# Performance work log

Hardware: AMD Instinct MI355X
Metric: run time of the kernel (lower is better)

The kernel has to match this reference:

```python
import jax, jax.numpy as jnp
import numpy as np

B, C, H, W = 8, 128, 64, 64

def setup_inputs() -> dict:
    key = jax.random.key(0)
    ks = jax.random.split(key, 7)
    s = 1.0 / np.sqrt(C)
    return {
        "x": jax.random.normal(ks[0], (B, C, H, W), dtype=jnp.float32),
        "Wq": jax.random.normal(ks[1], (C, C), dtype=jnp.float32) * s,
        "bq": jax.random.normal(ks[2], (C,), dtype=jnp.float32) * 0.01,
        "Wk": jax.random.normal(ks[3], (C, C), dtype=jnp.float32) * s,
        "bk": jax.random.normal(ks[4], (C,), dtype=jnp.float32) * 0.01,
        "Wv": jax.random.normal(ks[5], (C, C), dtype=jnp.float32) * s,
        "bv": jax.random.normal(ks[6], (C,), dtype=jnp.float32) * 0.01,
    }

def reference(x, Wq, bq, Wk, bk, Wv, bv):
    b, c, h, w = x.shape
    n = h * w
    scale = 1.0 / jnp.sqrt(jnp.asarray(c, x.dtype))
    xf = x.reshape(b, c, n)                                   # [B,C,N]
    # 1x1 convs == per-pixel linear layers
    q = jnp.einsum('oc,bcn->bno', Wq, xf) + bq                # [B,N,C]
    k = jnp.einsum('oc,bcn->bcn', Wk, xf) + bk[None, :, None] # [B,C,N]
    v = jnp.einsum('oc,bcn->bno', Wv, xf) + bv                # [B,N,C]
    attn = jax.nn.softmax(jnp.einsum('bnc,bcm->bnm', q, k) * scale, axis=-1)
    out = jnp.einsum('bnm,bmc->bnc', attn, v)                 # [B,N,C]
    return x + out.transpose(0, 2, 1).reshape(b, c, h, w)
```

## Files before the change

### kernel.cpp

```cpp
#include <hip/hip_runtime.h>

#define BB 8
#define CC 128
#define NN 4096

typedef __bf16 bf16x8_t __attribute__((ext_vector_type(8)));
typedef unsigned short u16x8 __attribute__((ext_vector_type(8)));
typedef float f32x4 __attribute__((ext_vector_type(4)));
typedef unsigned int u32x4 __attribute__((ext_vector_type(4)));
typedef __attribute__((address_space(1))) const unsigned int gu32;
typedef __attribute__((address_space(3))) unsigned int lu32;

#define KSCALE 0.12753262456033348f
#define MANCH  8.0f

__device__ __forceinline__ unsigned short f2bf(float f) {
  unsigned int u = __builtin_bit_cast(unsigned int, f);
  u += 0x7fffu + ((u >> 16) & 1u);
  return (unsigned short)(u >> 16);
}

__device__ __forceinline__ float bf2f(unsigned short s) {
  unsigned int u = ((unsigned int)s) << 16;
  return __builtin_bit_cast(float, u);
}

__device__ __forceinline__ unsigned int cvt_pk_bf16(float lo, float hi) {
  unsigned int r;
  asm("v_cvt_pk_bf16_f32 %0, %1, %2" : "=v"(r) : "v"(lo), "v"(hi));
  return r;
}

__device__ __forceinline__ float fexp2(float x) {
  float r;
  asm("v_exp_f32 %0, %1" : "=v"(r) : "v"(x));
  return r;
}

__device__ __forceinline__ f32x4 mfma16(u16x8 a, u16x8 b, f32x4 c) {
  return __builtin_amdgcn_mfma_f32_16x16x32_bf16(
      __builtin_bit_cast(bf16x8_t, a), __builtin_bit_cast(bf16x8_t, b), c, 0, 0, 0);
}

__global__ void prep(const float* __restrict__ Wq, const float* __restrict__ Wv,
                     const float* __restrict__ Wk,
                     unsigned short* __restrict__ Qwb, unsigned short* __restrict__ Vwb,
                     float* __restrict__ csk) {
  if (blockIdx.x < 64) {
    const int i = blockIdx.x * 256 + threadIdx.x;
    Qwb[i] = f2bf(Wq[i] * KSCALE);
    Vwb[i] = f2bf(Wv[i]);
  } else if (threadIdx.x < CC) {
    const int c = threadIdx.x;
    float s = 0.f;
    for (int o = 0; o < CC; ++o) s += Wk[(size_t)o * CC + c];
    csk[c] = s;
  }
}

__global__ __launch_bounds__(256, 2) void qkv_proj(
    const float* __restrict__ x,
    const unsigned short* __restrict__ Qwb, const float* __restrict__ bq,
    const float* __restrict__ csk, const float* __restrict__ bk,
    const unsigned short* __restrict__ Vwb, const float* __restrict__ bv,
    unsigned short* __restrict__ Q,
    unsigned short* __restrict__ K,
    unsigned short* __restrict__ V)
{
  const int b  = blockIdx.x & 7;
  const int n0 = (blockIdx.x >> 3) << 6;
  const int t  = threadIdx.x;
  const int lane = t & 63;
  const int w  = t >> 6;
  const int lq = lane & 15;
  const int g  = lane >> 4;

  __shared__ unsigned short xs[64][136];
  __shared__ unsigned short ks[64][136];
  __shared__ unsigned short vs[128][72];

  {
    const int n = t & 63;
    const float* xp = x + (size_t)b * (CC * NN) + n0 + n;
    for (int c = t >> 6; c < CC; c += 4) {
      const float xv = xp[(size_t)c * NN];
      xs[n][c] = f2bf(xv);
      ks[n][c] = f2bf(xv * csk[c] + bk[c]);
    }
  }
  __syncthreads();

  u16x8 a[4];
  {
    const unsigned short* ap = &xs[w * 16 + lq][g * 8];
    for (int ksl = 0; ksl < 4; ++ksl) a[ksl] = *(const u16x8*)(ap + ksl * 32);
  }

  for (int ot = 0; ot < 8; ++ot) {
    f32x4 aq = {0.f,0.f,0.f,0.f}, av = {0.f,0.f,0.f,0.f};
    const int o = ot * 16 + lq;
    const unsigned short* wq = Qwb + (size_t)o * CC + g * 8;
    const unsigned short* wv = Vwb + (size_t)o * CC + g * 8;
    for (int ksl = 0; ksl < 4; ++ksl) {
      aq = mfma16(a[ksl], *(const u16x8*)(wq + ksl * 32), aq);
      av = mfma16(a[ksl], *(const u16x8*)(wv + ksl * 32), av);
    }
    const float bqv = bq[o] * KSCALE, bvv = bv[o];
    for (int r = 0; r < 4; ++r) {
      const int nl = w * 16 + g * 4 + r;
      Q[((size_t)b * NN + n0 + nl) * CC + o] = f2bf(aq[r] + bqv);
      vs[o][nl] = f2bf(av[r] + bvv);
    }
  }
  __syncthreads();

  {
    unsigned short* kout = K + ((size_t)b * NN + n0) * CC;
    for (int i = t; i < 64 * 16; i += 256) {
      const int n = i >> 4, oc = (i & 15) * 8;
      *(uint4*)(kout + (size_t)n * CC + oc) = *(const uint4*)&ks[n][oc];
    }
  }
  {
    unsigned short* vout = V + (size_t)b * (CC * NN) + n0;
    for (int i = t; i < 128 * 32; i += 256) {
      const int c  = i >> 5;
      const int np = (i & 31) << 1;
      *(unsigned int*)(vout + (size_t)c * NN + np) = *(const unsigned int*)&vs[c][np];
    }
  }
}

__global__ __launch_bounds__(512, 4) void flash_attn(
    const unsigned short* __restrict__ Q,
    const unsigned short* __restrict__ K,
    const unsigned short* __restrict__ V,
    unsigned short* __restrict__ PO,
    float* __restrict__ PL)
{
  const int bid = blockIdx.x;
  const int b  = bid & 7;
  const int qb = (bid >> 3) & 31;
  const int sp = bid >> 8;
  const int kv0 = sp << 11;
  const int t  = threadIdx.x;
  const int lane = t & 63;
  const int w  = t >> 6;
  const int lq = lane & 15;
  const int g  = lane >> 4;
  const int q0w = (qb << 7) + (w << 4);

  __shared__ unsigned short KtL[2][64 * 128];
  __shared__ unsigned short VlL[2][128 * 64];

  u16x8 qf[4];
  {
    const unsigned short* qp = Q + ((size_t)b * NN + q0w + lq) * CC + g * 8;
    #pragma unroll
    for (int ksl = 0; ksl < 4; ++ksl) qf[ksl] = *(const u16x8*)(qp + ksl * 32);
  }

  const char* kgb = (const char*)(K + (size_t)b * NN * CC);
  const char* vgb = (const char*)(V + (size_t)b * CC * NN);
  int soK[2];
  #pragma unroll
  for (int j = 0; j < 2; ++j) {
    const int p = t * 16 + j * 8192;
    const int row = p >> 8;
    soK[j] = (p & ~255) | ((p & 255) ^ ((row & 15) << 4));
  }
  int vOff[8];
  #pragma unroll
  for (int n = 0; n < 8; ++n) {
    const int p = t * 4 + n * 2048;
    const int ch = p >> 7;
    const int L = (p & 127) ^ ((ch & 7) << 4);
    const int gb = (L & 7) | (((L >> 4) & 3) << 3) | (((L >> 3) & 1) << 5) | ((L >> 6) << 6);
    vOff[n] = ch * (NN * 2) + gb;
  }

  #define STAGE(nb, kv) do {                                                      \
    const char* kg_ = kgb + ((size_t)(kv) << 8);                                  \
    const char* vg_ = vgb + ((size_t)(kv) << 1);                                  \
    _Pragma("unroll")                                                             \
    for (int j = 0; j < 2; ++j)                                                   \
      __builtin_amdgcn_global_load_lds((gu32*)(kg_ + soK[j]),                     \
          (lu32*)((char*)KtL + (nb) * 16384 + t * 16 + j * 8192), 16, 0, 0);      \
    _Pragma("unroll")                                                             \
    for (int n = 0; n < 8; ++n)                                                   \
      __builtin_amdgcn_global_load_lds((gu32*)(vg_ + vOff[n]),                    \
          (lu32*)((char*)VlL + (nb) * 16384 + t * 4 + n * 2048), 4, 0, 0);        \
  } while (0)

  f32x4 oacc[8];
  #pragma unroll
  for (int i = 0; i < 8; ++i) oacc[i] = f32x4{0.f, 0.f, 0.f, 0.f};
  float l_run = 0.f;

  const int swzK  = lq << 4;
  const int swzVl = (lq & 7) << 4;

  STAGE(0, kv0);

  for (int tt = 0; tt < 32; ++tt) {
    const int cur = tt & 1;
    if (tt < 31) {
      STAGE(cur ^ 1, kv0 + (tt + 1) * 64);
      asm volatile("s_waitcnt vmcnt(10)" ::: "memory");
    } else {
      asm volatile("s_waitcnt vmcnt(0)" ::: "memory");
    }
    __builtin_amdgcn_s_barrier();

    const char* kb  = (const char*)KtL + cur * 16384;
    const char* vbb = (const char*)VlL + cur * 16384;

    f32x4 s[4];
    #pragma unroll
    for (int kt = 0; kt < 4; ++kt) s[kt] = f32x4{-MANCH, -MANCH, -MANCH, -MANCH};
    __builtin_amdgcn_s_setprio(1);
    #pragma unroll
    for (int kt = 0; kt < 4; ++kt) {
      const char* kp = kb + (kt * 16 + lq) * 256;
      #pragma unroll
      for (int ksl = 0; ksl < 4; ++ksl) {
        u16x8 kf = *(const u16x8*)(kp + ((ksl * 64 + g * 16) ^ swzK));
        s[kt] = mfma16(kf, qf[ksl], s[kt]);
      }
    }
    __builtin_amdgcn_s_setprio(0);

    #pragma unroll
    for (int kt = 0; kt < 4; ++kt) {
      s[kt][0] = fexp2(s[kt][0]); s[kt][1] = fexp2(s[kt][1]);
      s[kt][2] = fexp2(s[kt][2]); s[kt][3] = fexp2(s[kt][3]);
    }
    float lsum = 0.f;
    unsigned pkw[8];
    #pragma unroll
    for (int kt = 0; kt < 4; ++kt) {
      lsum += (s[kt][0] + s[kt][1]) + (s[kt][2] + s[kt][3]);
      pkw[kt * 2 + 0] = cvt_pk_bf16(s[kt][0], s[kt][1]);
      pkw[kt * 2 + 1] = cvt_pk_bf16(s[kt][2], s[kt][3]);
    }

    u32x4 pw0 = {pkw[0], pkw[1], pkw[2], pkw[3]};
    u32x4 pw1 = {pkw[4], pkw[5], pkw[6], pkw[7]};
    const u16x8 pf0 = __builtin_bit_cast(u16x8, pw0);
    const u16x8 pf1 = __builtin_bit_cast(u16x8, pw1);
    __builtin_amdgcn_s_setprio(1);
    #pragma unroll
    for (int dt = 0; dt < 8; ++dt) {
      const char* vp = vbb + (dt * 16 + lq) * 128;
      u16x8 vf0 = *(const u16x8*)(vp + ((g * 16) ^ swzVl));
      oacc[dt] = mfma16(vf0, pf0, oacc[dt]);
      u16x8 vf1 = *(const u16x8*)(vp + ((64 + g * 16) ^ swzVl));
      oacc[dt] = mfma16(vf1, pf1, oacc[dt]);
    }
    __builtin_amdgcn_s_setprio(0);

    lsum += __shfl_xor(lsum, 16);
    lsum += __shfl_xor(lsum, 32);
    l_run += lsum;

    asm volatile("s_waitcnt lgkmcnt(0)" ::: "memory");
    __builtin_amdgcn_s_barrier();
  }
  #undef STAGE

  const float rinv = 1.0f / l_run;
  const int n = q0w + lq;
  unsigned short* po = PO + (size_t)sp * (BB * CC * NN) + (size_t)b * (CC * NN);
  #pragma unroll
  for (int dt = 0; dt < 8; ++dt) {
    #pragma unroll
    for (int r = 0; r < 4; ++r) {
      const int c = dt * 16 + g * 4 + r;
      po[(size_t)c * NN + n] = f2bf(oacc[dt][r] * rinv);
    }
  }
  if (g == 0) PL[((size_t)sp * BB + b) * NN + n] = l_run;
}

__global__ __launch_bounds__(256) void combine(
    const float* __restrict__ x,
    const unsigned short* __restrict__ PO,
    const float* __restrict__ PL,
    float* __restrict__ out)
{
  const size_t base = ((size_t)blockIdx.x * 256 + threadIdx.x) * 4;
  const int n = (int)(base & 4095);
  const int b = (int)(base >> 19);
  const float l0 = PL[(size_t)b * NN + n];
  const float l1 = PL[(size_t)(BB + b) * NN + n];
  const float inv = 1.0f / (l0 + l1);
  const float w0 = l0 * inv, w1 = l1 * inv;

  ushort4 o0 = *(const ushort4*)(PO + base);
  ushort4 o1 = *(const ushort4*)(PO + (size_t)BB * CC * NN + base);
  float4 xv = *(const float4*)(x + base);
  float4 r;
  r.x = xv.x + w0 * bf2f(o0.x) + w1 * bf2f(o1.x);
  r.y = xv.y + w0 * bf2f(o0.y) + w1 * bf2f(o1.y);
  r.z = xv.z + w0 * bf2f(o0.z) + w1 * bf2f(o1.z);
  r.w = xv.w + w0 * bf2f(o0.w) + w1 * bf2f(o1.w);
  *(float4*)(out + base) = r;
}

extern "C" void kernel_launch(void* const* d_in, const int* in_sizes, int n_in,
                              void* d_out, int out_size, void* d_ws, size_t ws_size,
                              hipStream_t stream) {
  (void)in_sizes; (void)n_in; (void)out_size; (void)ws_size;
  const float* x  = (const float*)d_in[0];
  const float* Wq = (const float*)d_in[1];
  const float* bq = (const float*)d_in[2];
  const float* Wk = (const float*)d_in[3];
  const float* bk = (const float*)d_in[4];
  const float* Wv = (const float*)d_in[5];
  const float* bv = (const float*)d_in[6];

  unsigned short* Q   = (unsigned short*)d_ws;
  unsigned short* K   = Q + (size_t)BB * NN * CC;
  unsigned short* V   = K + (size_t)BB * NN * CC;
  unsigned short* PO  = V + (size_t)BB * NN * CC;
  float* PL           = (float*)(PO + (size_t)2 * BB * CC * NN);
  unsigned short* Qwb = (unsigned short*)(PL + (size_t)2 * BB * NN);
  unsigned short* Vwb = Qwb + (size_t)CC * CC;
  float* csk = (float*)(Vwb + (size_t)CC * CC);
  float* out = (float*)d_out;

  prep<<<dim3(65), dim3(256), 0, stream>>>(Wq, Wv, Wk, Qwb, Vwb, csk);
  qkv_proj<<<dim3(BB * (NN / 64)), dim3(256), 0, stream>>>(x, Qwb, bq, csk, bk, Vwb, bv, Q, K, V);
  flash_attn<<<dim3(BB * 32 * 2), dim3(512), 0, stream>>>(Q, K, V, PO, PL);
  combine<<<dim3((BB * CC * NN) / (256 * 4)), dim3(256), 0, stream>>>(x, PO, PL, out);
}
```

Baseline: 114.9 us.

## Switch flash attention to 32x32x16 MFMA tiles with 4 waves per block

Rewrites the attention inner loop to use 32x32x16 bf16 MFMA instead of 16x16x32. Each wave now owns 32 query rows, and blocks shrink to 256 threads. The V tile staging moves to 16-byte async loads with a new swizzle, and v_permlane32_swap reshapes the P fragments into the B operand layout. The aim is fewer MFMA issues, fewer LDS reads per FLOP and wider global-to-LDS transfers, at the cost of higher register pressure per wave and fewer waves available to hide latency.

```diff
diff --git a/kernel.cpp b/kernel.cpp
--- a/kernel.cpp
+++ b/kernel.cpp
@@ -7,6 +7,7 @@
 typedef __bf16 bf16x8_t __attribute__((ext_vector_type(8)));
 typedef unsigned short u16x8 __attribute__((ext_vector_type(8)));
 typedef float f32x4 __attribute__((ext_vector_type(4)));
+typedef float f32x16 __attribute__((ext_vector_type(16)));
 typedef unsigned int u32x4 __attribute__((ext_vector_type(4)));
 typedef __attribute__((address_space(1))) const unsigned int gu32;
 typedef __attribute__((address_space(3))) unsigned int lu32;
@@ -39,6 +40,11 @@
 
 __device__ __forceinline__ f32x4 mfma16(u16x8 a, u16x8 b, f32x4 c) {
   return __builtin_amdgcn_mfma_f32_16x16x32_bf16(
+      __builtin_bit_cast(bf16x8_t, a), __builtin_bit_cast(bf16x8_t, b), c, 0, 0, 0);
+}
+
+__device__ __forceinline__ f32x16 mfma32(u16x8 a, u16x8 b, f32x16 c) {
+  return __builtin_amdgcn_mfma_f32_32x32x16_bf16(
       __builtin_bit_cast(bf16x8_t, a), __builtin_bit_cast(bf16x8_t, b), c, 0, 0, 0);
 }
 
@@ -131,7 +137,7 @@
   }
 }
 
-__global__ __launch_bounds__(512, 4) void flash_attn(
+__global__ __launch_bounds__(256, 2) void flash_attn(
     const unsigned short* __restrict__ Q,
     const unsigned short* __restrict__ K,
     const unsigned short* __restrict__ V,
@@ -146,59 +152,56 @@
   const int t  = threadIdx.x;
   const int lane = t & 63;
   const int w  = t >> 6;
-  const int lq = lane & 15;
-  const int g  = lane >> 4;
-  const int q0w = (qb << 7) + (w << 4);
+  const int cl = lane & 31;
+  const int hi = lane >> 5;
+  const int q0w = (qb << 7) + (w << 5);
 
   __shared__ unsigned short KtL[2][64 * 128];
-  __shared__ unsigned short VlL[2][128 * 64];
-
-  u16x8 qf[4];
-  {
-    const unsigned short* qp = Q + ((size_t)b * NN + q0w + lq) * CC + g * 8;
-    #pragma unroll
-    for (int ksl = 0; ksl < 4; ++ksl) qf[ksl] = *(const u16x8*)(qp + ksl * 32);
+  __shared__ unsigned short VlL[2][64 * 128];
+
+  u16x8 qf[8];
+  {
+    const unsigned short* qp = Q + ((size_t)b * NN + q0w + cl) * CC + hi * 8;
+    #pragma unroll
+    for (int ks = 0; ks < 8; ++ks) qf[ks] = *(const u16x8*)(qp + ks * 16);
   }
 
   const char* kgb = (const char*)(K + (size_t)b * NN * CC);
   const char* vgb = (const char*)(V + (size_t)b * CC * NN);
-  int soK[2];
+  int soK[4], vOff[4];
   #pragma unroll
-  for (int j = 0; j < 2; ++j) {
-    const int p = t * 16 + j * 8192;
+  for (int j = 0; j < 4; ++j) {
+    const int p = t * 16 + j * 4096;
     const int row = p >> 8;
-    soK[j] = (p & ~255) | ((p & 255) ^ ((row & 15) << 4));
-  }
-  int vOff[8];
-  #pragma unroll
-  for (int n = 0; n < 8; ++n) {
-    const int p = t * 4 + n * 2048;
-    const int ch = p >> 7;
-    const int L = (p & 127) ^ ((ch & 7) << 4);
-    const int gb = (L & 7) | (((L >> 4) & 3) << 3) | (((L >> 3) & 1) << 5) | ((L >> 6) << 6);
-    vOff[n] = ch * (NN * 2) + gb;
+    const int L = (p & 255) ^ ((row & 15) << 4);
+    soK[j] = (p & ~255) | L;
+    const int ch = row * 2 + (L >> 7);
+    vOff[j] = ch * (NN * 2) + (L & 127);
   }
 
   #define STAGE(nb, kv) do {                                                      \
     const char* kg_ = kgb + ((size_t)(kv) << 8);                                  \
     const char* vg_ = vgb + ((size_t)(kv) << 1);                                  \
     _Pragma("unroll")                                                             \
-    for (int j = 0; j < 2; ++j)                                                   \
+    for (int j = 0; j < 4; ++j)                                                   \
       __builtin_amdgcn_global_load_lds((gu32*)(kg_ + soK[j]),                     \
-          (lu32*)((char*)KtL + (nb) * 16384 + t * 16 + j * 8192), 16, 0, 0);      \
+          (lu32*)((char*)KtL + (nb) * 16384 + t * 16 + j * 4096), 16, 0, 0);      \
     _Pragma("unroll")                                                             \
-    for (int n = 0; n < 8; ++n)                                                   \
-      __builtin_amdgcn_global_load_lds((gu32*)(vg_ + vOff[n]),                    \
-          (lu32*)((char*)VlL + (nb) * 16384 + t * 4 + n * 2048), 4, 0, 0);        \
+    for (int j = 0; j < 4; ++j)                                                   \
+      __builtin_amdgcn_global_load_lds((gu32*)(vg_ + vOff[j]),                    \
+          (lu32*)((char*)VlL + (nb) * 16384 + t * 16 + j * 4096), 16, 0, 0);      \
   } while (0)
 
-  f32x4 oacc[8];
+  f32x16 oacc[4];
   #pragma unroll
-  for (int i = 0; i < 8; ++i) oacc[i] = f32x4{0.f, 0.f, 0.f, 0.f};
+  for (int i = 0; i < 4; ++i)
+    #pragma unroll
+    for (int r = 0; r < 16; ++r) oacc[i][r] = 0.f;
   float l_run = 0.f;
 
-  const int swzK  = lq << 4;
-  const int swzVl = (lq & 7) << 4;
+  const int swzK = (cl & 15) << 4;
+  const int swzV = ((cl >> 1) & 15) << 4;
+  const int vbase = (cl & 1) << 7;
 
   STAGE(0, kv0);
 
@@ -206,7 +209,7 @@
     const int cur = tt & 1;
     if (tt < 31) {
       STAGE(cur ^ 1, kv0 + (tt + 1) * 64);
-      asm volatile("s_waitcnt vmcnt(10)" ::: "memory");
+      asm volatile("s_waitcnt vmcnt(8)" ::: "memory");
     } else {
       asm volatile("s_waitcnt vmcnt(0)" ::: "memory");
     }
@@ -215,51 +218,78 @@
     const char* kb  = (const char*)KtL + cur * 16384;
     const char* vbb = (const char*)VlL + cur * 16384;
 
-    f32x4 s[4];
-    #pragma unroll
-    for (int kt = 0; kt < 4; ++kt) s[kt] = f32x4{-MANCH, -MANCH, -MANCH, -MANCH};
+    f32x16 s0, s1;
+    #pragma unroll
+    for (int r = 0; r < 16; ++r) { s0[r] = -MANCH; s1[r] = -MANCH; }
+    const char* kp0 = kb + cl * 256;
+    const char* kp1 = kb + (32 + cl) * 256;
     __builtin_amdgcn_s_setprio(1);
     #pragma unroll
-    for (int kt = 0; kt < 4; ++kt) {
-      const char* kp = kb + (kt * 16 + lq) * 256;
+    for (int ks = 0; ks < 8; ++ks) {
+      const int off = (ks * 32 + hi * 16) ^ swzK;
+      u16x8 kf0 = *(const u16x8*)(kp0 + off);
+      s0 = mfma32(kf0, qf[ks], s0);
+      u16x8 kf1 = *(const u16x8*)(kp1 + off);
+      s1 = mfma32(kf1, qf[ks], s1);
+    }
+    __builtin_amdgcn_s_setprio(0);
+
+    float lsum = 0.f;
+
+    #pragma unroll
+    for (int r = 0; r < 16; ++r) { s0[r] = fexp2(s0[r]); lsum += s0[r]; }
+    {
+      unsigned pk0 = cvt_pk_bf16(s0[0],  s0[1]),  pk1 = cvt_pk_bf16(s0[2],  s0[3]);
+      unsigned pk2 = cvt_pk_bf16(s0[4],  s0[5]),  pk3 = cvt_pk_bf16(s0[6],  s0[7]);
+      unsigned pk4 = cvt_pk_bf16(s0[8],  s0[9]),  pk5 = cvt_pk_bf16(s0[10], s0[11]);
+      unsigned pk6 = cvt_pk_bf16(s0[12], s0[13]), pk7 = cvt_pk_bf16(s0[14], s0[15]);
+      asm("v_permlane32_swap_b32 %0, %1" : "+v"(pk0), "+v"(pk2));
+      asm("v_permlane32_swap_b32 %0, %1" : "+v"(pk1), "+v"(pk3));
+      asm("v_permlane32_swap_b32 %0, %1" : "+v"(pk4), "+v"(pk6));
+      asm("v_permlane32_swap_b32 %0, %1" : "+v"(pk5), "+v"(pk7));
+      u32x4 pw0 = {pk0, pk1, pk2, pk3};
+      u32x4 pw1 = {pk4, pk5, pk6, pk7};
+      const u16x8 pf0 = __builtin_bit_cast(u16x8, pw0);
+      const u16x8 pf1 = __builtin_bit_cast(u16x8, pw1);
+      __builtin_amdgcn_s_setprio(1);
       #pragma unroll
-      for (int ksl = 0; ksl < 4; ++ksl) {
-        u16x8 kf = *(const u16x8*)(kp + ((ksl * 64 + g * 16) ^ swzK));
-        s[kt] = mfma16(kf, qf[ksl], s[kt]);
+      for (int ct = 0; ct < 4; ++ct) {
+        const char* vp = vbb + (ct * 16 + (cl >> 1)) * 256;
+        u16x8 vf0 = *(const u16x8*)(vp + ((vbase + 0  + hi * 16) ^ swzV));
+        oacc[ct] = mfma32(vf0, pf0, oacc[ct]);
+        u16x8 vf1 = *(const u16x8*)(vp + ((vbase + 32 + hi * 16) ^ swzV));
+        oacc[ct] = mfma32(vf1, pf1, oacc[ct]);
       }
-    }
-    __builtin_amdgcn_s_setprio(0);
-
-    #pragma unroll
-    for (int kt = 0; kt < 4; ++kt) {
-      s[kt][0] = fexp2(s[kt][0]); s[kt][1] = fexp2(s[kt][1]);
-      s[kt][2] = fexp2(s[kt][2]); s[kt][3] = fexp2(s[kt][3]);
-    }
-    float lsum = 0.f;
-    unsigned pkw[8];
-    #pragma unroll
-    for (int kt = 0; kt < 4; ++kt) {
-      lsum += (s[kt][0] + s[kt][1]) + (s[kt][2] + s[kt][3]);
-      pkw[kt * 2 + 0] = cvt_pk_bf16(s[kt][0], s[kt][1]);
-      pkw[kt * 2 + 1] = cvt_pk_bf16(s[kt][2], s[kt][3]);
-    }
-
-    u32x4 pw0 = {pkw[0], pkw[1], pkw[2], pkw[3]};
-    u32x4 pw1 = {pkw[4], pkw[5], pkw[6], pkw[7]};
-    const u16x8 pf0 = __builtin_bit_cast(u16x8, pw0);
-    const u16x8 pf1 = __builtin_bit_cast(u16x8, pw1);
-    __builtin_amdgcn_s_setprio(1);
-    #pragma unroll
-    for (int dt = 0; dt < 8; ++dt) {
-      const char* vp = vbb + (dt * 16 + lq) * 128;
-      u16x8 vf0 = *(const u16x8*)(vp + ((g * 16) ^ swzVl));
-      oacc[dt] = mfma16(vf0, pf0, oacc[dt]);
-      u16x8 vf1 = *(const u16x8*)(vp + ((64 + g * 16) ^ swzVl));
-      oacc[dt] = mfma16(vf1, pf1, oacc[dt]);
-    }
-    __builtin_amdgcn_s_setprio(0);
-
-    lsum += __shfl_xor(lsum, 16);
+      __builtin_amdgcn_s_setprio(0);
+    }
+
+    #pragma unroll
+    for (int r = 0; r < 16; ++r) { s1[r] = fexp2(s1[r]); lsum += s1[r]; }
+    {
+      unsigned pk0 = cvt_pk_bf16(s1[0],  s1[1]),  pk1 = cvt_pk_bf16(s1[2],  s1[3]);
+      unsigned pk2 = cvt_pk_bf16(s1[4],  s1[5]),  pk3 = cvt_pk_bf16(s1[6],  s1[7]);
+      unsigned pk4 = cvt_pk_bf16(s1[8],  s1[9]),  pk5 = cvt_pk_bf16(s1[10], s1[11]);
+      unsigned pk6 = cvt_pk_bf16(s1[12], s1[13]), pk7 = cvt_pk_bf16(s1[14], s1[15]);
+      asm("v_permlane32_swap_b32 %0, %1" : "+v"(pk0), "+v"(pk2));
+      asm("v_permlane32_swap_b32 %0, %1" : "+v"(pk1), "+v"(pk3));
+      asm("v_permlane32_swap_b32 %0, %1" : "+v"(pk4), "+v"(pk6));
+      asm("v_permlane32_swap_b32 %0, %1" : "+v"(pk5), "+v"(pk7));
+      u32x4 pw0 = {pk0, pk1, pk2, pk3};
+      u32x4 pw1 = {pk4, pk5, pk6, pk7};
+      const u16x8 pf0 = __builtin_bit_cast(u16x8, pw0);
+      const u16x8 pf1 = __builtin_bit_cast(u16x8, pw1);
+      __builtin_amdgcn_s_setprio(1);
+      #pragma unroll
+      for (int ct = 0; ct < 4; ++ct) {
+        const char* vp = vbb + (ct * 16 + (cl >> 1)) * 256;
+        u16x8 vf0 = *(const u16x8*)(vp + ((vbase + 64 + hi * 16) ^ swzV));
+        oacc[ct] = mfma32(vf0, pf0, oacc[ct]);
+        u16x8 vf1 = *(const u16x8*)(vp + ((vbase + 96 + hi * 16) ^ swzV));
+        oacc[ct] = mfma32(vf1, pf1, oacc[ct]);
+      }
+      __builtin_amdgcn_s_setprio(0);
+    }
+
     lsum += __shfl_xor(lsum, 32);
     l_run += lsum;
 
@@ -269,17 +299,16 @@
   #undef STAGE
 
   const float rinv = 1.0f / l_run;
-  const int n = q0w + lq;
+  const int n = q0w + cl;
   unsigned short* po = PO + (size_t)sp * (BB * CC * NN) + (size_t)b * (CC * NN);
   #pragma unroll
-  for (int dt = 0; dt < 8; ++dt) {
-    #pragma unroll
-    for (int r = 0; r < 4; ++r) {
-      const int c = dt * 16 + g * 4 + r;
-      po[(size_t)c * NN + n] = f2bf(oacc[dt][r] * rinv);
-    }
-  }
-  if (g == 0) PL[((size_t)sp * BB + b) * NN + n] = l_run;
+  for (int ct = 0; ct < 4; ++ct)
+    #pragma unroll
+    for (int r = 0; r < 16; ++r) {
+      const int c = ct * 32 + (r & 3) + 8 * (r >> 2) + 4 * hi;
+      po[(size_t)c * NN + n] = f2bf(oacc[ct][r] * rinv);
+    }
+  if (hi == 0) PL[((size_t)sp * BB + b) * NN + n] = l_run;
 }
 
 __global__ __launch_bounds__(256) void combine(
@@ -331,6 +360,6 @@
 
   prep<<<dim3(65), dim3(256), 0, stream>>>(Wq, Wv, Wk, Qwb, Vwb, csk);
   qkv_proj<<<dim3(BB * (NN / 64)), dim3(256), 0, stream>>>(x, Qwb, bq, csk, bk, Vwb, bv, Q, K, V);
-  flash_attn<<<dim3(BB * 32 * 2), dim3(512), 0, stream>>>(Q, K, V, PO, PL);
+  flash_attn<<<dim3(BB * 32 * 2), dim3(256), 0, stream>>>(Q, K, V, PO, PL);
   combine<<<dim3((BB * CC * NN) / (256 * 4)), dim3(256), 0, stream>>>(x, PO, PL, out);
 }
```

After: 111.4 us. 1.03x faster.
